# Kernel optimization log

Measured on AMD Instinct MI355X. Metric: run time of the kernel, lower is better.

The kernel has to match this reference:

```python
import jax, jax.numpy as jnp
import numpy as np
from itertools import combinations_with_replacement

IN_FEATURES = 128
ORDER = 3
BIAS = True
WEIGHT_DIVISOR = 100.0
BATCH = 256


def _make_comb_idx():
    n_feat = IN_FEATURES + (1 if BIAS else 0)  # 129
    idx = np.array(list(combinations_with_replacement(range(n_feat), ORDER)), dtype=np.int32)
    return jnp.asarray(idx)  # [num_combinations, ORDER] = [366145, 3]


def setup_inputs() -> dict:
    key = jax.random.key(0)
    kx, kw = jax.random.split(key)
    x = jax.random.normal(kx, (BATCH, IN_FEATURES), dtype=jnp.float32)
    comb_idx = _make_comb_idx()
    num_weights = comb_idx.shape[0]
    weight = jax.random.uniform(kw, (num_weights,), dtype=jnp.float32) / WEIGHT_DIVISOR
    return {"x": x, "weight": weight, "comb_idx": comb_idx}


def reference(x, weight, comb_idx):
    # Prepend bias column of ones: xb [B, in_features+1]
    ones = jnp.ones((x.shape[0], 1), dtype=x.dtype)
    xb = jnp.concatenate([ones, x], axis=1)
    # Gather per-combination features: [B, num_combinations, ORDER]
    gathered = xb[:, comb_idx]
    # Monomial products: [B, num_combinations]
    colx = jnp.prod(gathered, axis=2)
    # Weighted sum -> [B, 1]; activation is identity
    return colx @ weight[:, None]
```

## Files before the change

kernel.cpp:

```cpp
#include <hip/hip_runtime.h>


#define NF      129
#define NCOMB   366145
#define NPAIR   8385
#define NT      4
#define NCHUNK  132
#define NKS     4

typedef short bf16x8 __attribute__((ext_vector_type(8)));
typedef float f32x4  __attribute__((ext_vector_type(4)));

static __device__ inline unsigned bfpack2(float lo, float hi) {
    union { float f; unsigned u; } a, b; a.f = lo; b.f = hi;
    return ((b.u + 0x8000u) & 0xffff0000u) | ((a.u + 0x8000u) >> 16);
}

static __device__ inline void dpair(int p, int& i0, int& i1) {
    int t = (int)((259.0f - sqrtf((float)(67081 - 8 * p))) * 0.5f);
    t = t < 0 ? 0 : (t > 128 ? 128 : t);
    while (t < 128 && ((t + 1) * (258 - t)) / 2 <= p) ++t;
    while (t > 0   && (t * (259 - t)) / 2      >  p) --t;
    i0 = t; i1 = t + (p - (t * (259 - t)) / 2);
}

static __device__ inline int mbase(int i0, int i1) {
    const int n0 = NF - i0, n1 = NF - i1;
    return NCOMB - (n0 * (n0 + 1) * (n0 + 2)) / 6
                 + ((n0 * (n0 + 1)) >> 1) - ((n1 * (n1 + 1)) >> 1);
}

__global__ __launch_bounds__(256, 3) void honu_fused(const float* __restrict__ x,
                                                     const float* __restrict__ w,
                                                     float* __restrict__ out) {
    __shared__ char   uA[64 * NF * 4];
    __shared__ bf16x8 wls[NT * NKS * 64];
    __shared__ int4   dec[64];
    float*          xf   = (float*)uA;
    unsigned short* slab = (unsigned short*)uA;

    const int tid  = threadIdx.x;
    const int lane = tid & 63;
    const int wv   = tid >> 6;
    const int bx   = blockIdx.x;
    const int by   = blockIdx.y;

    const int p0 = bx * 64;
    int a0, a1; dpair(p0, a0, a1);
    const int mstart = mbase(a0, a1);
    int mend = NCOMB;
    if (p0 + 64 < NPAIR) { int b0, b1; dpair(p0 + 64, b0, b1); mend = mbase(b0, b1); }
    const int L = mend - mstart;

    float4 xreg[8];
    {
        const int r = tid >> 2, q = tid & 3;
        const float4* xrp = (const float4*)(x + (size_t)(by * 64 + r) * 128);
        #pragma unroll
        for (int t = 0; t < 8; ++t) xreg[t] = xrp[q + 4 * t];
    }

    if (tid < 64) {
        const int p = p0 + tid;
        int i0 = 0, i1 = 200, mb = 0, bo = 0; unsigned wl = 0;
        if (p < NPAIR) {
            dpair(p, i0, i1);
            mb = mbase(i0, i1);
            bo = mb - mstart - i1;
            union { float f; unsigned u; } c; c.f = w[mb + 128 - i1];
            wl = c.u;
        }
        dec[tid] = make_int4(i0 | (i1 << 16), mb, (int)wl, bo);
    }

    for (int i = tid * 2; i < L; i += 512) {
        const float lo = w[mstart + i];
        const float hi = (i + 1 < L) ? w[mstart + i + 1] : 0.0f;
        ((unsigned*)slab)[i >> 1] = bfpack2(lo, hi);
    }
    __syncthreads();

    #pragma unroll
    for (int it = 0; it < 4; ++it) {
        const int item = tid + it * 256;
        const int pl = item >> 4, r = item & 15;
        const int4 pd = dec[pl];
        const int i1 = pd.x >> 16;
        const int bo = pd.w;
        const int k0 = r * 8;
        int4 vout = make_int4(0, 0, 0, 0);
        if (k0 + 7 >= i1) {
            unsigned sv[8];
            #pragma unroll
            for (int j = 0; j < 8; ++j) {
                const int k = k0 + j;
                int ad = bo + k; ad = ad < 0 ? 0 : ad;
                const unsigned t = slab[ad];
                sv[j] = (k >= i1) ? t : 0u;
            }
            vout.x = (int)(sv[0] | (sv[1] << 16));
            vout.y = (int)(sv[2] | (sv[3] << 16));
            vout.z = (int)(sv[4] | (sv[5] << 16));
            vout.w = (int)(sv[6] | (sv[7] << 16));
        }
        const int nt = pl >> 4, s = r >> 2;
        const int slane = ((r & 3) << 4) | (pl & 15);
        ((int4*)wls)[(nt * NKS + s) * 64 + slane] = vout;
    }
    __syncthreads();

    {
        const int r = tid >> 2, q = tid & 3;
        #pragma unroll
        for (int t = 0; t < 8; ++t) {
            const int c4 = q + 4 * t;
            float* d = &xf[r * NF + 1 + 4 * c4];
            d[0] = xreg[t].x; d[1] = xreg[t].y; d[2] = xreg[t].z; d[3] = xreg[t].w;
        }
        if (tid < 64) xf[tid * NF] = 1.0f;
    }
    __syncthreads();

    const int am = wv * 16 + (lane & 15);
    const int aq = (lane >> 4) * 8;
    const float* xa = &xf[am * NF + aq];
    bf16x8 a[NKS];
    #pragma unroll
    for (int s = 0; s < NKS; ++s) {
        const float* p = xa + s * 32;
        union { int4 i; bf16x8 b; } av;
        av.i.x = (int)bfpack2(p[0], p[1]);
        av.i.y = (int)bfpack2(p[2], p[3]);
        av.i.z = (int)bfpack2(p[4], p[5]);
        av.i.w = (int)bfpack2(p[6], p[7]);
        a[s] = av.b;
    }

    const int lr0 = wv * 16 + (lane >> 4) * 4;
    const float* r0 = &xf[lr0 * NF];
    float o0 = 0.f, o1 = 0.f, o2 = 0.f, o3 = 0.f;

    #pragma unroll
    for (int nt = 0; nt < NT; ++nt) {
        f32x4 acc = {0.f, 0.f, 0.f, 0.f};
        #pragma unroll
        for (int s = 0; s < NKS; ++s)
            acc = __builtin_amdgcn_mfma_f32_16x16x32_bf16(
                      a[s], wls[(nt * NKS + s) * 64 + lane], acc, 0, 0, 0);

        const int4 pd = dec[nt * 16 + (lane & 15)];
        const int i0 = pd.x & 0xffff;
        int i1 = pd.x >> 16; if (i1 > 128) i1 = 0;
        union { int i; float f; } wc; wc.i = pd.z;
        const float wl = wc.f;
        o0 = fmaf(acc[0] + r0[128]          * wl, r0[i0]          * r0[i1],          o0);
        o1 = fmaf(acc[1] + r0[NF + 128]     * wl, r0[NF + i0]     * r0[NF + i1],     o1);
        o2 = fmaf(acc[2] + r0[2 * NF + 128] * wl, r0[2 * NF + i0] * r0[2 * NF + i1], o2);
        o3 = fmaf(acc[3] + r0[3 * NF + 128] * wl, r0[3 * NF + i0] * r0[3 * NF + i1], o3);
    }

    #pragma unroll
    for (int msk = 1; msk < 16; msk <<= 1) {
        o0 += __shfl_xor(o0, msk);
        o1 += __shfl_xor(o1, msk);
        o2 += __shfl_xor(o2, msk);
        o3 += __shfl_xor(o3, msk);
    }
    if ((lane & 15) == 0) {
        float* po = out + by * 64 + lr0;
        atomicAdd(po + 0, o0);
        atomicAdd(po + 1, o1);
        atomicAdd(po + 2, o2);
        atomicAdd(po + 3, o3);
    }
}

extern "C" void kernel_launch(void* const* d_in, const int* in_sizes, int n_in,
                              void* d_out, int out_size, void* d_ws, size_t ws_size,
                              hipStream_t stream) {
    const float* x      = (const float*)d_in[0];
    const float* weight = (const float*)d_in[1];
    float* out = (float*)d_out;

    honu_fused<<<dim3(NCHUNK, 4), 256, 0, stream>>>(x, weight, out);
}
```

Measured before the change: 78.07 us.

## Process whole batch per block with 48-pair chunks across 176 blocks

Replaces the 2D grid (pair chunks × batch quarters) with a 1D grid where each 512-thread block holds all 256 batch rows in shared memory and handles 48 pairs. Each weight slab is now loaded and bf16-converted once instead of four times, and the per-pair linear weight is read from the slab instead of a separate global load. In exchange, every block loads the full x matrix into about 132KB of LDS, which limits it to one block per CU, and the x staging is no longer overlapped with other work.

```diff
diff --git a/kernel.cpp b/kernel.cpp
--- a/kernel.cpp
+++ b/kernel.cpp
@@ -4,9 +4,10 @@
 #define NF      129
 #define NCOMB   366145
 #define NPAIR   8385
-#define NT      4
-#define NCHUNK  132
+#define NT      3
+#define NBLK    176
 #define NKS     4
+#define WRAWSZ  5120
 
 typedef short bf16x8 __attribute__((ext_vector_type(8)));
 typedef float f32x4  __attribute__((ext_vector_type(4)));
@@ -30,63 +31,61 @@
                  + ((n0 * (n0 + 1)) >> 1) - ((n1 * (n1 + 1)) >> 1);
 }
 
-__global__ __launch_bounds__(256, 3) void honu_fused(const float* __restrict__ x,
+__global__ __launch_bounds__(512, 1) void honu_fused(const float* __restrict__ x,
                                                      const float* __restrict__ w,
                                                      float* __restrict__ out) {
-    __shared__ char   uA[64 * NF * 4];
-    __shared__ bf16x8 wls[NT * NKS * 64];
-    __shared__ int4   dec[64];
-    float*          xf   = (float*)uA;
-    unsigned short* slab = (unsigned short*)uA;
+    __shared__ float          xf[256 * NF];
+    __shared__ bf16x8         wls[NT * NKS * 64];
+    __shared__ unsigned short slab[WRAWSZ];
+    __shared__ int4           dec[NT * 16];
 
     const int tid  = threadIdx.x;
     const int lane = tid & 63;
     const int wv   = tid >> 6;
     const int bx   = blockIdx.x;
-    const int by   = blockIdx.y;
 
-    const int p0 = bx * 64;
+    const int p0 = bx * (NT * 16);
     int a0, a1; dpair(p0, a0, a1);
     const int mstart = mbase(a0, a1);
     int mend = NCOMB;
-    if (p0 + 64 < NPAIR) { int b0, b1; dpair(p0 + 64, b0, b1); mend = mbase(b0, b1); }
+    if (p0 + NT * 16 < NPAIR) { int b0, b1; dpair(p0 + NT * 16, b0, b1); mend = mbase(b0, b1); }
     const int L = mend - mstart;
 
-    float4 xreg[8];
-    {
-        const int r = tid >> 2, q = tid & 3;
-        const float4* xrp = (const float4*)(x + (size_t)(by * 64 + r) * 128);
-        #pragma unroll
-        for (int t = 0; t < 8; ++t) xreg[t] = xrp[q + 4 * t];
-    }
-
-    if (tid < 64) {
-        const int p = p0 + tid;
-        int i0 = 0, i1 = 200, mb = 0, bo = 0; unsigned wl = 0;
-        if (p < NPAIR) {
-            dpair(p, i0, i1);
-            mb = mbase(i0, i1);
-            bo = mb - mstart - i1;
-            union { float f; unsigned u; } c; c.f = w[mb + 128 - i1];
-            wl = c.u;
-        }
-        dec[tid] = make_int4(i0 | (i1 << 16), mb, (int)wl, bo);
-    }
-
-    for (int i = tid * 2; i < L; i += 512) {
+    for (int i = tid * 2; i < L; i += 1024) {
         const float lo = w[mstart + i];
         const float hi = (i + 1 < L) ? w[mstart + i + 1] : 0.0f;
         ((unsigned*)slab)[i >> 1] = bfpack2(lo, hi);
     }
+
+    {
+        const float4* xv = (const float4*)x;
+        #pragma unroll 8
+        for (int t = 0; t < 16; ++t) {
+            const int f = tid + t * 512;
+            const int r = f >> 5, c4 = f & 31;
+            const float4 v = xv[f];
+            float* d = &xf[r * NF + 1 + 4 * c4];
+            d[0] = v.x; d[1] = v.y; d[2] = v.z; d[3] = v.w;
+        }
+        if (tid < 256) xf[tid * NF] = 1.0f;
+    }
+
+    if (tid < NT * 16) {
+        const int p = p0 + tid;
+        int i0 = 0, i1 = 200, bo = 0;
+        if (p < NPAIR) {
+            dpair(p, i0, i1);
+            bo = mbase(i0, i1) - mstart - i1;
+        }
+        dec[tid] = make_int4(i0 | (i1 << 16), bo, 0, 0);
+    }
     __syncthreads();
 
-    #pragma unroll
-    for (int it = 0; it < 4; ++it) {
-        const int item = tid + it * 256;
+    for (int item = tid; item < NT * 256; item += 512) {
         const int pl = item >> 4, r = item & 15;
         const int4 pd = dec[pl];
         const int i1 = pd.x >> 16;
-        const int bo = pd.w;
+        const int bo = pd.y;
         const int k0 = r * 8;
         int4 vout = make_int4(0, 0, 0, 0);
         if (k0 + 7 >= i1) {
@@ -109,69 +108,63 @@
     }
     __syncthreads();
 
-    {
-        const int r = tid >> 2, q = tid & 3;
+    for (int mt = wv; mt < 16; mt += 8) {
+        const int am = mt * 16 + (lane & 15);
+        const int aq = (lane >> 4) * 8;
+        const float* xa = &xf[am * NF + aq];
+        bf16x8 a[NKS];
         #pragma unroll
-        for (int t = 0; t < 8; ++t) {
-            const int c4 = q + 4 * t;
-            float* d = &xf[r * NF + 1 + 4 * c4];
-            d[0] = xreg[t].x; d[1] = xreg[t].y; d[2] = xreg[t].z; d[3] = xreg[t].w;
+        for (int s = 0; s < NKS; ++s) {
+            const float* p = xa + s * 32;
+            union { int4 i; bf16x8 b; } av;
+            av.i.x = (int)bfpack2(p[0], p[1]);
+            av.i.y = (int)bfpack2(p[2], p[3]);
+            av.i.z = (int)bfpack2(p[4], p[5]);
+            av.i.w = (int)bfpack2(p[6], p[7]);
+            a[s] = av.b;
         }
-        if (tid < 64) xf[tid * NF] = 1.0f;
-    }
-    __syncthreads();
 
-    const int am = wv * 16 + (lane & 15);
-    const int aq = (lane >> 4) * 8;
-    const float* xa = &xf[am * NF + aq];
-    bf16x8 a[NKS];
-    #pragma unroll
-    for (int s = 0; s < NKS; ++s) {
-        const float* p = xa + s * 32;
-        union { int4 i; bf16x8 b; } av;
-        av.i.x = (int)bfpack2(p[0], p[1]);
-        av.i.y = (int)bfpack2(p[2], p[3]);
-        av.i.z = (int)bfpack2(p[4], p[5]);
-        av.i.w = (int)bfpack2(p[6], p[7]);
-        a[s] = av.b;
-    }
+        const int lr0 = mt * 16 + (lane >> 4) * 4;
+        const float* r0 = &xf[lr0 * NF];
+        float o0 = 0.f, o1 = 0.f, o2 = 0.f, o3 = 0.f;
 
-    const int lr0 = wv * 16 + (lane >> 4) * 4;
-    const float* r0 = &xf[lr0 * NF];
-    float o0 = 0.f, o1 = 0.f, o2 = 0.f, o3 = 0.f;
+        #pragma unroll
+        for (int nt = 0; nt < NT; ++nt) {
+            f32x4 acc = {0.f, 0.f, 0.f, 0.f};
+            #pragma unroll
+            for (int s = 0; s < NKS; ++s)
+                acc = __builtin_amdgcn_mfma_f32_16x16x32_bf16(
+                          a[s], wls[(nt * NKS + s) * 64 + lane], acc, 0, 0, 0);
 
-    #pragma unroll
-    for (int nt = 0; nt < NT; ++nt) {
-        f32x4 acc = {0.f, 0.f, 0.f, 0.f};
+            const int4 pd = dec[nt * 16 + (lane & 15)];
+            const int i0 = pd.x & 0xffff;
+            int i1 = pd.x >> 16;
+            float wl = 0.0f;
+            if (i1 <= 128) {
+                union { unsigned u; float f; } c;
+                c.u = ((unsigned)slab[pd.y + 128]) << 16;
+                wl = c.f;
+            } else i1 = 0;
+            o0 = fmaf(acc[0] + r0[128]          * wl, r0[i0]          * r0[i1],          o0);
+            o1 = fmaf(acc[1] + r0[NF + 128]     * wl, r0[NF + i0]     * r0[NF + i1],     o1);
+            o2 = fmaf(acc[2] + r0[2 * NF + 128] * wl, r0[2 * NF + i0] * r0[2 * NF + i1], o2);
+            o3 = fmaf(acc[3] + r0[3 * NF + 128] * wl, r0[3 * NF + i0] * r0[3 * NF + i1], o3);
+        }
+
         #pragma unroll
-        for (int s = 0; s < NKS; ++s)
-            acc = __builtin_amdgcn_mfma_f32_16x16x32_bf16(
-                      a[s], wls[(nt * NKS + s) * 64 + lane], acc, 0, 0, 0);
-
-        const int4 pd = dec[nt * 16 + (lane & 15)];
-        const int i0 = pd.x & 0xffff;
-        int i1 = pd.x >> 16; if (i1 > 128) i1 = 0;
-        union { int i; float f; } wc; wc.i = pd.z;
-        const float wl = wc.f;
-        o0 = fmaf(acc[0] + r0[128]          * wl, r0[i0]          * r0[i1],          o0);
-        o1 = fmaf(acc[1] + r0[NF + 128]     * wl, r0[NF + i0]     * r0[NF + i1],     o1);
-        o2 = fmaf(acc[2] + r0[2 * NF + 128] * wl, r0[2 * NF + i0] * r0[2 * NF + i1], o2);
-        o3 = fmaf(acc[3] + r0[3 * NF + 128] * wl, r0[3 * NF + i0] * r0[3 * NF + i1], o3);
-    }
-
-    #pragma unroll
-    for (int msk = 1; msk < 16; msk <<= 1) {
-        o0 += __shfl_xor(o0, msk);
-        o1 += __shfl_xor(o1, msk);
-        o2 += __shfl_xor(o2, msk);
-        o3 += __shfl_xor(o3, msk);
-    }
-    if ((lane & 15) == 0) {
-        float* po = out + by * 64 + lr0;
-        atomicAdd(po + 0, o0);
-        atomicAdd(po + 1, o1);
-        atomicAdd(po + 2, o2);
-        atomicAdd(po + 3, o3);
+        for (int msk = 1; msk < 16; msk <<= 1) {
+            o0 += __shfl_xor(o0, msk);
+            o1 += __shfl_xor(o1, msk);
+            o2 += __shfl_xor(o2, msk);
+            o3 += __shfl_xor(o3, msk);
+        }
+        if ((lane & 15) == 0) {
+            float* po = out + lr0;
+            atomicAdd(po + 0, o0);
+            atomicAdd(po + 1, o1);
+            atomicAdd(po + 2, o2);
+            atomicAdd(po + 3, o3);
+        }
     }
 }
 
@@ -182,5 +175,5 @@
     const float* weight = (const float*)d_in[1];
     float* out = (float*)d_out;
 
-    honu_fused<<<dim3(NCHUNK, 4), 256, 0, stream>>>(x, weight, out);
+    honu_fused<<<NBLK, 512, 0, stream>>>(x, weight, out);
 }
```

New measurement: 81.80 us. +4.8%, slower.
